# Kernel tuning notes

Hardware: AMD Instinct MI355X
Metric: run time of the kernel (lower is better)

Reference implementation:

```python
import jax, jax.numpy as jnp
import numpy as np

BN_EPS = 1e-5
NN_EPS = 1e-8
K = 3


def conv_bn_relu(x, W, b, gamma, beta, mean, var):
    # x: [B, Cin, N]; W: [Cout, Cin] (1x1 conv); BN in inference mode w/ running stats
    y = jnp.einsum('bcn,oc->bon', x, W) + b[None, :, None]
    y = (y - mean[None, :, None]) * (gamma / jnp.sqrt(var + BN_EPS))[None, :, None] + beta[None, :, None]
    return jax.nn.relu(y)


def three_interpolation(p1, p2, f2):
    # p1: [B, N1, 3] unknown xyz; p2: [B, N2, 3] known xyz; f2: [B, C, N2]
    # squared pairwise distances via the expansion trick (avoids [B,N1,N2,3])
    d2 = (jnp.sum(p1 * p1, -1)[:, :, None]
          + jnp.sum(p2 * p2, -1)[:, None, :]
          - 2.0 * jnp.einsum('bnd,bmd->bnm', p1, p2))  # [B, N1, N2]
    neg_d2, idx = jax.lax.top_k(-d2, K)                 # 3 nearest
    dist = -neg_d2                                      # squared dists, [B, N1, 3]
    recip = 1.0 / (dist + NN_EPS)
    weight = recip / jnp.sum(recip, axis=-1, keepdims=True)  # [B, N1, 3]
    f2t = jnp.transpose(f2, (0, 2, 1))                  # [B, N2, C]
    gathered = jax.vmap(lambda f, i: f[i])(f2t, idx)    # [B, N1, 3, C]
    return jnp.einsum('bnkc,bnk->bcn', gathered, weight)  # [B, C, N1]


def setup_inputs() -> dict:
    key = jax.random.key(0)
    ks = jax.random.split(key, 16)
    B, N1, N2 = 8, 16384, 4096
    mlp = [256, 128, 128]
    inp = {
        'p1': jax.random.normal(ks[0], (B, N1, 3), jnp.float32),
        'p2': jax.random.normal(ks[1], (B, N2, 3), jnp.float32),
        'f2': jax.random.normal(ks[2], (B, mlp[0], N2), jnp.float32),
    }
    kidx = 3
    for li in range(len(mlp) - 1):
        cin, cout = mlp[li], mlp[li + 1]
        inp[f'W{li}'] = jax.random.normal(ks[kidx], (cout, cin), jnp.float32) * (1.0 / np.sqrt(cin)); kidx += 1
        inp[f'b{li}'] = jnp.zeros((cout,), jnp.float32)
        inp[f'gamma{li}'] = jnp.ones((cout,), jnp.float32)
        inp[f'beta{li}'] = jnp.zeros((cout,), jnp.float32)
        inp[f'mean{li}'] = jax.random.normal(ks[kidx], (cout,), jnp.float32) * 0.1; kidx += 1
        inp[f'var{li}'] = jax.random.uniform(ks[kidx], (cout,), jnp.float32, 0.5, 1.5); kidx += 1
    return inp


def reference(p1, p2, f2,
              W0, b0, gamma0, beta0, mean0, var0,
              W1, b1, gamma1, beta1, mean1, var1):
    f = conv_bn_relu(f2, W0, b0, gamma0, beta0, mean0, var0)
    f = conv_bn_relu(f, W1, b1, gamma1, beta1, mean1, var1)
    return three_interpolation(p1, p2, f)
```

## Files before the change

kernel.cpp:

```cpp
#include <hip/hip_runtime.h>

#define B_    8
#define N1_   16384
#define N2_   4096
#define NTOT_ (B_ * N1_)

__device__ __forceinline__ float np_sumsq(float x, float y, float z)
{
#pragma clang fp contract(off)
    return ((x * x + y * y) + z * z);
}

__global__ __launch_bounds__(256) void fold_kernel(
    const float* __restrict__ W, const float* __restrict__ bias,
    const float* __restrict__ gamma, const float* __restrict__ beta,
    const float* __restrict__ mean, const float* __restrict__ var,
    float* __restrict__ Wp, float* __restrict__ bp, int Cout, int Cin)
{
    int t = blockIdx.x * 256 + threadIdx.x;
    if (t < Cout * Cin) {
        int o = t / Cin;
        float s = gamma[o] / sqrtf(var[o] + 1e-5f);
        Wp[t] = W[t] * s;
    }
    if (t < Cout) {
        float s = gamma[t] / sqrtf(var[t] + 1e-5f);
        bp[t] = beta[t] + (bias[t] - mean[t]) * s;
    }
}

__global__ __launch_bounds__(256) void q4_kernel(
    const float* __restrict__ p2, float4* __restrict__ q4)
{
    int t = blockIdx.x * 256 + threadIdx.x;
    float x = p2[3 * (size_t)t + 0];
    float y = p2[3 * (size_t)t + 1];
    float z = p2[3 * (size_t)t + 2];
    q4[t] = make_float4(x, y, z, np_sumsq(x, y, z));
}

template <int CIN, bool TRANS>
__global__ __launch_bounds__(256) void gemm_relu_kernel(
    const float* __restrict__ X, const float* __restrict__ Wp,
    const float* __restrict__ bp, float* __restrict__ Y)
{
    __shared__ float A_lds[32][136];
    __shared__ float B_lds[32][128];

    const int b  = blockIdx.y;
    const int n0 = blockIdx.x * 128;
    const int tid = threadIdx.x;
    const int ty = tid >> 4;
    const int tx = tid & 15;
    const float* Xb = X + (size_t)b * CIN * N2_;

    float acc[8][8];
#pragma unroll
    for (int i = 0; i < 8; ++i)
#pragma unroll
        for (int j = 0; j < 8; ++j) acc[i][j] = 0.f;

    const int ka = tid & 31, mb = (tid >> 5) * 16;
    const int nb = tid & 127, kb = (tid >> 7) * 16;

    for (int k0 = 0; k0 < CIN; k0 += 32) {
#pragma unroll
        for (int i = 0; i < 16; ++i)
            A_lds[ka][mb + i] = Wp[(size_t)(mb + i) * CIN + k0 + ka];
#pragma unroll
        for (int i = 0; i < 16; ++i)
            B_lds[kb + i][nb] = Xb[(size_t)(k0 + kb + i) * N2_ + n0 + nb];
        __syncthreads();

#pragma unroll
        for (int kk = 0; kk < 32; ++kk) {
            const float4 a0 = *(const float4*)&A_lds[kk][ty * 4];
            const float4 a1 = *(const float4*)&A_lds[kk][64 + ty * 4];
            const float4 bq0 = *(const float4*)&B_lds[kk][tx * 4];
            const float4 bq1 = *(const float4*)&B_lds[kk][64 + tx * 4];
            const float av[8] = {a0.x, a0.y, a0.z, a0.w, a1.x, a1.y, a1.z, a1.w};
            const float bv[8] = {bq0.x, bq0.y, bq0.z, bq0.w, bq1.x, bq1.y, bq1.z, bq1.w};
#pragma unroll
            for (int i = 0; i < 8; ++i)
#pragma unroll
                for (int j = 0; j < 8; ++j)
                    acc[i][j] = fmaf(av[i], bv[j], acc[i][j]);
        }
        __syncthreads();
    }

    float bias_v[8];
#pragma unroll
    for (int i = 0; i < 8; ++i) {
        const int r = (i < 4) ? (ty * 4 + i) : (64 + ty * 4 + (i - 4));
        bias_v[i] = bp[r];
    }

    if (!TRANS) {
#pragma unroll
        for (int i = 0; i < 8; ++i) {
            const int r = (i < 4) ? (ty * 4 + i) : (64 + ty * 4 + (i - 4));
            float* yrow = Y + ((size_t)b * 128 + r) * N2_ + n0;
            float4 v0, v1;
            v0.x = fmaxf(acc[i][0] + bias_v[i], 0.f);
            v0.y = fmaxf(acc[i][1] + bias_v[i], 0.f);
            v0.z = fmaxf(acc[i][2] + bias_v[i], 0.f);
            v0.w = fmaxf(acc[i][3] + bias_v[i], 0.f);
            v1.x = fmaxf(acc[i][4] + bias_v[i], 0.f);
            v1.y = fmaxf(acc[i][5] + bias_v[i], 0.f);
            v1.z = fmaxf(acc[i][6] + bias_v[i], 0.f);
            v1.w = fmaxf(acc[i][7] + bias_v[i], 0.f);
            *(float4*)(yrow + tx * 4) = v0;
            *(float4*)(yrow + 64 + tx * 4) = v1;
        }
    } else {
#pragma unroll
        for (int j = 0; j < 8; ++j) {
            const int c = (j < 4) ? (tx * 4 + j) : (64 + tx * 4 + (j - 4));
            float* ycol = Y + ((size_t)b * N2_ + n0 + c) * 128;
            float4 v0, v1;
            v0.x = fmaxf(acc[0][j] + bias_v[0], 0.f);
            v0.y = fmaxf(acc[1][j] + bias_v[1], 0.f);
            v0.z = fmaxf(acc[2][j] + bias_v[2], 0.f);
            v0.w = fmaxf(acc[3][j] + bias_v[3], 0.f);
            v1.x = fmaxf(acc[4][j] + bias_v[4], 0.f);
            v1.y = fmaxf(acc[5][j] + bias_v[5], 0.f);
            v1.z = fmaxf(acc[6][j] + bias_v[6], 0.f);
            v1.w = fmaxf(acc[7][j] + bias_v[7], 0.f);
            *(float4*)(ycol + ty * 4) = v0;
            *(float4*)(ycol + 64 + ty * 4) = v1;
        }
    }
}

__global__ __launch_bounds__(256, 6) void knn_phase1(
    const float* __restrict__ p1, const float4* __restrict__ q4,
    float* __restrict__ part_d, int* __restrict__ part_i)
{
    __shared__ float4 qs[1024];
    const int tid = threadIdx.x;
    const int chunk = blockIdx.x & 3;
    const int g = (blockIdx.x >> 2) * 256 + tid;
    const int b = g >> 14;

    const float px = p1[3 * (size_t)g + 0];
    const float py = p1[3 * (size_t)g + 1];
    const float pz = p1[3 * (size_t)g + 2];
    const float s1 = np_sumsq(px, py, pz);

    const float4* qb = q4 + (size_t)b * N2_ + chunk * 1024;
#pragma unroll
    for (int i = 0; i < 4; ++i) qs[tid + i * 256] = qb[tid + i * 256];
    __syncthreads();

    float d0 = 1e30f, d1 = 1e30f, d2v = 1e30f;
    int i0 = 0, i1 = 0, i2 = 0;
    const int jbase = chunk * 1024;

    for (int j = 0; j < 1024; j += 4) {
#pragma unroll
        for (int u = 0; u < 4; ++u) {
            const float4 q = qs[j + u];
            const float dot = __fmaf_rn(px, q.x, __fmaf_rn(py, q.y, __fmul_rn(pz, q.z)));
            const float ss  = s1 + q.w;
            const float t   = __fmaf_rn(-2.0f, dot, ss);
            if (t < d2v) {
                const int jj = jbase + j + u;
                const bool c1 = t < d1, c0 = t < d0;
                d2v = c1 ? d1 : t;                 i2 = c1 ? i1 : jj;
                const float nd1 = c1 ? (c0 ? d0 : t) : d1;
                const int   ni1 = c1 ? (c0 ? i0 : jj) : i1;
                d1 = nd1;                          i1 = ni1;
                d0 = c0 ? t : d0;                  i0 = c0 ? jj : i0;
            }
        }
    }

    part_d[(0 * 4 + chunk) * NTOT_ + g] = d0;
    part_d[(1 * 4 + chunk) * NTOT_ + g] = d1;
    part_d[(2 * 4 + chunk) * NTOT_ + g] = d2v;
    part_i[(0 * 4 + chunk) * NTOT_ + g] = i0;
    part_i[(1 * 4 + chunk) * NTOT_ + g] = i1;
    part_i[(2 * 4 + chunk) * NTOT_ + g] = i2;
}

__global__ __launch_bounds__(256) void knn_merge(
    const float* __restrict__ part_d, const int* __restrict__ part_i,
    int* __restrict__ idx_ws, float* __restrict__ w_ws)
{
    const int g = blockIdx.x * 256 + threadIdx.x;

    float d0 = 1e30f, d1 = 1e30f, d2v = 1e30f;
    int i0 = 0, i1 = 0, i2 = 0;

#pragma unroll
    for (int c = 0; c < 4; ++c) {
#pragma unroll
        for (int k = 0; k < 3; ++k) {
            const float t = part_d[(k * 4 + c) * NTOT_ + g];
            const int  jj = part_i[(k * 4 + c) * NTOT_ + g];
            if (t < d2v) {
                const bool c1 = t < d1, c0 = t < d0;
                d2v = c1 ? d1 : t;                 i2 = c1 ? i1 : jj;
                const float nd1 = c1 ? (c0 ? d0 : t) : d1;
                const int   ni1 = c1 ? (c0 ? i0 : jj) : i1;
                d1 = nd1;                          i1 = ni1;
                d0 = c0 ? t : d0;                  i0 = c0 ? jj : i0;
            }
        }
    }

    float w0, w1, w2;
    {
#pragma clang fp contract(off)
        const float r0 = 1.0f / (d0 + 1e-8f);
        const float r1 = 1.0f / (d1 + 1e-8f);
        const float r2 = 1.0f / (d2v + 1e-8f);
        const float rs = (r0 + r1) + r2;
        w0 = r0 / rs;
        w1 = r1 / rs;
        w2 = r2 / rs;
    }

    idx_ws[g]             = i0;
    idx_ws[NTOT_ + g]     = i1;
    idx_ws[2 * NTOT_ + g] = i2;
    w_ws[g]               = w0;
    w_ws[NTOT_ + g]       = w1;
    w_ws[2 * NTOT_ + g]   = w2;
}

__global__ __launch_bounds__(256) void gather_kernel(
    const float* __restrict__ f_t, const int* __restrict__ idx_ws,
    const float* __restrict__ w_ws, float* __restrict__ out)
{
    const int tid = threadIdx.x;
    const int lane = tid & 63, cg = tid >> 6;
    const int g = blockIdx.x * 64 + lane;
    const int b = g >> 14, n = g & 16383;

    const int i0 = idx_ws[g];
    const int i1 = idx_ws[NTOT_ + g];
    const int i2 = idx_ws[2 * NTOT_ + g];
    const float w0 = w_ws[g];
    const float w1 = w_ws[NTOT_ + g];
    const float w2 = w_ws[2 * NTOT_ + g];

    const float* base = f_t + (size_t)b * N2_ * 128 + cg * 32;
    const float4* r0 = (const float4*)(base + (size_t)i0 * 128);
    const float4* r1 = (const float4*)(base + (size_t)i1 * 128);
    const float4* r2 = (const float4*)(base + (size_t)i2 * 128);

    float acc[32];
#pragma unroll
    for (int q = 0; q < 8; ++q) {
        const float4 a = r0[q], bb = r1[q], c = r2[q];
        acc[4 * q + 0] = fmaf(w0, a.x, fmaf(w1, bb.x, w2 * c.x));
        acc[4 * q + 1] = fmaf(w0, a.y, fmaf(w1, bb.y, w2 * c.y));
        acc[4 * q + 2] = fmaf(w0, a.z, fmaf(w1, bb.z, w2 * c.z));
        acc[4 * q + 3] = fmaf(w0, a.w, fmaf(w1, bb.w, w2 * c.w));
    }

    float* ob = out + ((size_t)b * 128 + cg * 32) * N1_ + n;
#pragma unroll
    for (int c = 0; c < 32; ++c) ob[(size_t)c * N1_] = acc[c];
}

extern "C" void kernel_launch(void* const* d_in, const int* in_sizes, int n_in,
                              void* d_out, int out_size, void* d_ws, size_t ws_size,
                              hipStream_t stream)
{
    const float* p1  = (const float*)d_in[0];
    const float* p2  = (const float*)d_in[1];
    const float* f2  = (const float*)d_in[2];
    const float* W0  = (const float*)d_in[3];
    const float* b0  = (const float*)d_in[4];
    const float* g0  = (const float*)d_in[5];
    const float* be0 = (const float*)d_in[6];
    const float* m0  = (const float*)d_in[7];
    const float* v0  = (const float*)d_in[8];
    const float* W1  = (const float*)d_in[9];
    const float* b1  = (const float*)d_in[10];
    const float* g1  = (const float*)d_in[11];
    const float* be1 = (const float*)d_in[12];
    const float* m1  = (const float*)d_in[13];
    const float* v1  = (const float*)d_in[14];

    char* ws = (char*)d_ws;
    float4* q4  = (float4*)(ws);
    float*  W0p = (float*)(ws + (512 << 10));
    float*  b0p = (float*)(ws + (640 << 10));
    float*  W1p = (float*)(ws + (644 << 10));
    float*  b1p = (float*)(ws + (708 << 10));
    float*  h   = (float*)(ws + ((size_t)1 << 20));
    float*  f_t = (float*)(ws + ((size_t)17 << 20));
    int*    idxw= (int*)  (ws + ((size_t)33 << 20));
    float*  wgt = (float*)(ws + ((size_t)35 << 20));
    float*  pd  = (float*)(ws + ((size_t)1 << 20));
    int*    pi  = (int*)  (ws + ((size_t)9 << 20));

    fold_kernel<<<128, 256, 0, stream>>>(W0, b0, g0, be0, m0, v0, W0p, b0p, 128, 256);
    fold_kernel<<<64, 256, 0, stream>>>(W1, b1, g1, be1, m1, v1, W1p, b1p, 128, 128);
    q4_kernel<<<(B_ * N2_) / 256, 256, 0, stream>>>(p2, q4);

    gemm_relu_kernel<256, false><<<dim3(32, 8), 256, 0, stream>>>(f2, W0p, b0p, h);
    gemm_relu_kernel<128, true ><<<dim3(32, 8), 256, 0, stream>>>(h, W1p, b1p, f_t);

    knn_phase1<<<(NTOT_ / 256) * 4, 256, 0, stream>>>(p1, q4, pd, pi);
    knn_merge<<<NTOT_ / 256, 256, 0, stream>>>(pd, pi, idxw, wgt);
    gather_kernel<<<NTOT_ / 64, 256, 0, stream>>>(f_t, idxw, wgt, (float*)d_out);
}
```

Measured before the change: 353.5 us.

## Vectorize GEMM tile loads, stage transposed output through LDS, tweak knn occupancy

The conv GEMM now loads its W and X tiles with float4 global reads instead of scalar strided reads. The transposed epilogue now stages results through shared memory in four 32-column slices, so each output row is written as coalesced float4 stores. Separately, knn_phase1's launch bounds rise from 6 to 8 blocks per CU, and the interpolation output uses nontemporal stores. In exchange, the epilogue adds extra barriers and LDS traffic, and the higher occupancy target may force register spills in the knn kernel.

After: 352.6 us. No clear change (-0.3%).

```diff
diff --git a/kernel.cpp b/kernel.cpp
--- a/kernel.cpp
+++ b/kernel.cpp
@@ -60,16 +60,27 @@
 #pragma unroll
         for (int j = 0; j < 8; ++j) acc[i][j] = 0.f;
 
-    const int ka = tid & 31, mb = (tid >> 5) * 16;
-    const int nb = tid & 127, kb = (tid >> 7) * 16;
+    const int a_kq = (tid & 7) * 4;
+    const int a_r0 = tid >> 3;
+    const int b_n4 = (tid & 31) * 4;
+    const int b_k0 = tid >> 5;
 
     for (int k0 = 0; k0 < CIN; k0 += 32) {
 #pragma unroll
-        for (int i = 0; i < 16; ++i)
-            A_lds[ka][mb + i] = Wp[(size_t)(mb + i) * CIN + k0 + ka];
-#pragma unroll
-        for (int i = 0; i < 16; ++i)
-            B_lds[kb + i][nb] = Xb[(size_t)(k0 + kb + i) * N2_ + n0 + nb];
+        for (int i = 0; i < 4; ++i) {
+            const int row = a_r0 + 32 * i;
+            const float4 v = *(const float4*)&Wp[(size_t)row * CIN + k0 + a_kq];
+            A_lds[a_kq + 0][row] = v.x;
+            A_lds[a_kq + 1][row] = v.y;
+            A_lds[a_kq + 2][row] = v.z;
+            A_lds[a_kq + 3][row] = v.w;
+        }
+#pragma unroll
+        for (int i = 0; i < 4; ++i) {
+            const int krow = b_k0 + 8 * i;
+            *(float4*)&B_lds[krow][b_n4] =
+                *(const float4*)&Xb[(size_t)(k0 + krow) * N2_ + n0 + b_n4];
+        }
         __syncthreads();
 
 #pragma unroll
@@ -114,26 +125,34 @@
             *(float4*)(yrow + 64 + tx * 4) = v1;
         }
     } else {
-#pragma unroll
-        for (int j = 0; j < 8; ++j) {
-            const int c = (j < 4) ? (tx * 4 + j) : (64 + tx * 4 + (j - 4));
-            float* ycol = Y + ((size_t)b * N2_ + n0 + c) * 128;
-            float4 v0, v1;
-            v0.x = fmaxf(acc[0][j] + bias_v[0], 0.f);
-            v0.y = fmaxf(acc[1][j] + bias_v[1], 0.f);
-            v0.z = fmaxf(acc[2][j] + bias_v[2], 0.f);
-            v0.w = fmaxf(acc[3][j] + bias_v[3], 0.f);
-            v1.x = fmaxf(acc[4][j] + bias_v[4], 0.f);
-            v1.y = fmaxf(acc[5][j] + bias_v[5], 0.f);
-            v1.z = fmaxf(acc[6][j] + bias_v[6], 0.f);
-            v1.w = fmaxf(acc[7][j] + bias_v[7], 0.f);
-            *(float4*)(ycol + ty * 4) = v0;
-            *(float4*)(ycol + 64 + ty * 4) = v1;
-        }
-    }
-}
-
-__global__ __launch_bounds__(256, 6) void knn_phase1(
+        float (*T)[132] = (float(*)[132])&A_lds[0][0];
+#pragma unroll
+        for (int s = 0; s < 4; ++s) {
+            if ((tx >> 3) == (s & 1)) {
+                const int joff = (s >> 1) * 4;
+                const int cl0 = (tx & 7) * 4;
+#pragma unroll
+                for (int i = 0; i < 8; ++i) {
+                    const int r = (i < 4) ? (ty * 4 + i) : (64 + ty * 4 + (i - 4));
+#pragma unroll
+                    for (int j = 0; j < 4; ++j)
+                        T[cl0 + j][r] = fmaxf(acc[i][j + joff] + bias_v[i], 0.f);
+                }
+            }
+            __syncthreads();
+#pragma unroll
+            for (int p = 0; p < 4; ++p) {
+                const int row = (tid >> 5) + 8 * p;
+                const float4 v = *(const float4*)&T[row][(tid & 31) * 4];
+                float* orow = Y + ((size_t)b * N2_ + n0 + 32 * s + row) * 128;
+                *(float4*)&orow[(tid & 31) * 4] = v;
+            }
+            __syncthreads();
+        }
+    }
+}
+
+__global__ __launch_bounds__(256, 8) void knn_phase1(
     const float* __restrict__ p1, const float4* __restrict__ q4,
     float* __restrict__ part_d, int* __restrict__ part_i)
 {
@@ -263,7 +282,8 @@
 
     float* ob = out + ((size_t)b * 128 + cg * 32) * N1_ + n;
 #pragma unroll
-    for (int c = 0; c < 32; ++c) ob[(size_t)c * N1_] = acc[c];
+    for (int c = 0; c < 32; ++c)
+        __builtin_nontemporal_store(acc[c], ob + (size_t)c * N1_);
 }
 
 extern "C" void kernel_launch(void* const* d_in, const int* in_sizes, int n_in,
```
